# Performance work log

Measured on AMD Instinct MI355X. Metric: run time of the kernel, lower is better.

Reference implementation:

```python
import jax, jax.numpy as jnp
import numpy as np


def setup_inputs() -> dict:
    key = jax.random.key(0)
    k1, k2, k3, k4 = jax.random.split(key, 4)
    B, T, S, D = 256, 16, 32, 768
    return {
        "video_global": jax.random.normal(k1, (B, D), dtype=jnp.float32),
        "text_global": jax.random.normal(k2, (B, D), dtype=jnp.float32),
        "video_local": jax.random.normal(k3, (B, T, D), dtype=jnp.float32),
        "text_local": jax.random.normal(k4, (B, S, D), dtype=jnp.float32),
        "temp": jnp.zeros((1,), dtype=jnp.float32),  # log(1.0)
    }


def reference(video_global, text_global, video_local, text_local, temp):
    B = video_global.shape[0]
    logit_scale = jnp.exp(temp)[0]

    # ---- global contrastive loss ----
    global_sim = logit_scale * (video_global @ text_global.T)  # [B, B]
    diag = jnp.arange(B)
    loss_v2t = -jax.nn.log_softmax(global_sim, axis=1)[diag, diag].mean()
    loss_t2v = -jax.nn.log_softmax(global_sim, axis=0)[diag, diag].mean()
    loss_global = 0.5 * (loss_v2t + loss_t2v)

    # ---- local positive scores ----
    # paired (diagonal) local similarity: [B, T, S]
    sim_pos = logit_scale * jnp.einsum("btd,bsd->bts", video_local, text_local)
    time_weights = jax.nn.softmax(sim_pos.max(axis=-1), axis=-1)  # [B, T]
    pos_scores = (sim_pos.mean(axis=-1) * time_weights).sum(axis=1)  # [B]

    # ---- local negative scores (batched pairwise contraction) ----
    # [B, B, T, S]: video i vs text j, replacing the B*(B-1) tiny einsum loop
    sim_all = logit_scale * jnp.einsum("btd,csd->bcts", video_local, text_local)
    neg_full = (time_weights[:, None, :] * sim_all.mean(axis=-1)).sum(axis=-1)  # [B, B]

    # drop diagonal (i == j), preserving row-major loop order
    rows, cols = np.nonzero(~np.eye(B, dtype=bool))
    neg_scores = neg_full[rows, cols].reshape(B, B - 1)

    logits = jnp.concatenate([pos_scores[:, None], neg_scores], axis=-1)  # [B, B]
    loss_local = -jax.nn.log_softmax(logits, axis=-1)[:, 0].mean()

    return 0.6 * loss_global + 0.4 * loss_local
```

## Files before the change

### kernel.cpp

```cpp
#include <hip/hip_runtime.h>
#include <cmath>

#define BB 256
#define TT 16
#define SS 32
#define DD 768
#define LROW 260

__global__ __launch_bounds__(512) void hl_stage1(
    const float* __restrict__ vl, const float* __restrict__ tl,
    const float* __restrict__ temp,
    float* __restrict__ vw_ws, float* __restrict__ tb_ws)
{
    __shared__ float smem[12480];
    __shared__ float simb[512];
    __shared__ float rmax[16];
    __shared__ float twb[16];

    const int i   = blockIdx.x;
    const int tid = threadIdx.x;
    const float lsc = expf(temp[0]);

    const int slice = tid & 15;
    const int g     = tid >> 4;
    const int tg    = g >> 3;
    const int sg    = g & 7;

    const float* vli = vl + (size_t)i * TT * DD;
    const float* tli = tl + (size_t)i * SS * DD;

    float acc[4][4];
#pragma unroll
    for (int a = 0; a < 4; ++a)
#pragma unroll
        for (int b = 0; b < 4; ++b) acc[a][b] = 0.f;

    for (int c = 0; c < 3; ++c) {
        const int d0 = c << 8;
#pragma unroll
        for (int k = 0; k < 2; ++k) {
            int f4 = tid + (k << 9);
            int r  = f4 >> 6;
            int dc = (f4 & 63) << 2;
            *(float4*)&smem[r * LROW + dc] = *(const float4*)&vli[r * DD + d0 + dc];
        }
#pragma unroll
        for (int k = 0; k < 4; ++k) {
            int f4 = tid + (k << 9);
            int r  = f4 >> 6;
            int dc = (f4 & 63) << 2;
            *(float4*)&smem[(16 + r) * LROW + dc] = *(const float4*)&tli[r * DD + d0 + dc];
        }
        __syncthreads();
#pragma unroll
        for (int step = 0; step < 4; ++step) {
            const int db = (slice << 4) + (step << 2);
            float4 av[4], bv[4];
#pragma unroll
            for (int ti = 0; ti < 4; ++ti)
                av[ti] = *(const float4*)&smem[(tg * 4 + ti) * LROW + db];
#pragma unroll
            for (int sj = 0; sj < 4; ++sj)
                bv[sj] = *(const float4*)&smem[(16 + sg * 4 + sj) * LROW + db];
#pragma unroll
            for (int ti = 0; ti < 4; ++ti)
#pragma unroll
                for (int sj = 0; sj < 4; ++sj)
                    acc[ti][sj] += av[ti].x * bv[sj].x + av[ti].y * bv[sj].y
                                 + av[ti].z * bv[sj].z + av[ti].w * bv[sj].w;
        }
        __syncthreads();
    }

#pragma unroll
    for (int ti = 0; ti < 4; ++ti)
#pragma unroll
        for (int sj = 0; sj < 4; ++sj) {
            int t = tg * 4 + ti, s = sg * 4 + sj;
            smem[(t * 32 + s) * 17 + slice] = acc[ti][sj];
        }
    __syncthreads();
    {
        float ssum = 0.f;
#pragma unroll
        for (int k = 0; k < 16; ++k) ssum += smem[tid * 17 + k];
        simb[tid] = lsc * ssum;
    }
    __syncthreads();
    if (tid < 16) {
        float m = -3.0e38f;
        for (int s = 0; s < 32; ++s)
            m = fmaxf(m, simb[tid * 32 + ((s + tid) & 31)]);
        rmax[tid] = m;
    }
    __syncthreads();
    if (tid == 0) {
        float M = -3.0e38f;
        for (int t = 0; t < 16; ++t) M = fmaxf(M, rmax[t]);
        float ssum = 0.f;
        for (int t = 0; t < 16; ++t) {
            float e = expf(rmax[t] - M);
            twb[t] = e;
            ssum += e;
        }
        float inv = 1.0f / ssum;
        for (int t = 0; t < 16; ++t) twb[t] *= inv;
    }
    __syncthreads();

    for (int d = tid; d < DD; d += 512) {
        float vwv = 0.f;
#pragma unroll
        for (int t = 0; t < 16; ++t) vwv += twb[t] * vli[t * DD + d];
        vw_ws[(size_t)i * DD + d] = vwv;
        float tbv = 0.f;
#pragma unroll
        for (int s = 0; s < 32; ++s) tbv += tli[s * DD + d];
        tb_ws[(size_t)i * DD + d] = tbv * (1.0f / 32.0f);
    }
}

__global__ __launch_bounds__(256) void hl_gemm(
    const float* __restrict__ vg, const float* __restrict__ tg,
    const float* __restrict__ vw, const float* __restrict__ tb,
    const float* __restrict__ temp, float* __restrict__ cparts)
{
    __shared__ float As[16][68];
    __shared__ float Bs[16][68];
    __shared__ float Tb[64][68];

    const int b   = blockIdx.x;
    const int p   = b & 7;
    const int tj  = (b >> 3) & 3;
    const int ti  = (b >> 5) & 3;
    const int mat = b >> 7;
    const int tid = threadIdx.x;
    const float lsc = expf(temp[0]);

    const float* A  = mat ? vw : vg;
    const float* Bm = mat ? tb : tg;
    const int i0 = ti * 64, j0 = tj * 64, kb0 = p * 96;

    const int srow = tid >> 2, skq = tid & 3;
    const int tr = tid >> 4, tc = tid & 15;

    float acc[4][4];
#pragma unroll
    for (int r = 0; r < 4; ++r)
#pragma unroll
        for (int cc = 0; cc < 4; ++cc) acc[r][cc] = 0.f;

    for (int ch = 0; ch < 6; ++ch) {
        const int kb = kb0 + ch * 16;
        float4 a4 = *(const float4*)&A [(size_t)(i0 + srow) * DD + kb + skq * 4];
        float4 b4 = *(const float4*)&Bm[(size_t)(j0 + srow) * DD + kb + skq * 4];
        __syncthreads();
        As[skq * 4 + 0][srow] = a4.x; As[skq * 4 + 1][srow] = a4.y;
        As[skq * 4 + 2][srow] = a4.z; As[skq * 4 + 3][srow] = a4.w;
        Bs[skq * 4 + 0][srow] = b4.x; Bs[skq * 4 + 1][srow] = b4.y;
        Bs[skq * 4 + 2][srow] = b4.z; Bs[skq * 4 + 3][srow] = b4.w;
        __syncthreads();
#pragma unroll
        for (int k = 0; k < 16; ++k) {
            float4 av = *(const float4*)&As[k][tr * 4];
            float4 bv = *(const float4*)&Bs[k][tc * 4];
            float ar[4] = {av.x, av.y, av.z, av.w};
            float br[4] = {bv.x, bv.y, bv.z, bv.w};
#pragma unroll
            for (int r = 0; r < 4; ++r)
#pragma unroll
                for (int cc = 0; cc < 4; ++cc)
                    acc[r][cc] += ar[r] * br[cc];
        }
    }

    const int cm = mat ? 0 : 1;
    float* Cp = cparts + ((size_t)p * 3 + cm) * 65536;
#pragma unroll
    for (int r = 0; r < 4; ++r) {
        float4 v = {acc[r][0] * lsc, acc[r][1] * lsc, acc[r][2] * lsc, acc[r][3] * lsc};
        *(float4*)&Cp[(size_t)(i0 + tr * 4 + r) * 256 + j0 + tc * 4] = v;
    }
    if (mat == 0) {
        __syncthreads();
#pragma unroll
        for (int r = 0; r < 4; ++r)
#pragma unroll
            for (int cc = 0; cc < 4; ++cc)
                Tb[tc * 4 + cc][tr * 4 + r] = acc[r][cc] * lsc;
        __syncthreads();
        float* Ct = cparts + ((size_t)p * 3 + 2) * 65536;
#pragma unroll
        for (int r = 0; r < 4; ++r) {
            float4 v = *(const float4*)&Tb[tr * 4 + r][tc * 4];
            *(float4*)&Ct[(size_t)(j0 + tr * 4 + r) * 256 + i0 + tc * 4] = v;
        }
    }
}

__global__ __launch_bounds__(256) void hl_lse(
    const float* __restrict__ cparts, float* __restrict__ out)
{
    __shared__ float xs[256];
    __shared__ float wred[4];
    __shared__ float bcast;

    const int b   = blockIdx.x;
    const int cm  = b >> 8;
    const int row = b & 255;
    const int tid = threadIdx.x;

    float x = 0.f;
#pragma unroll
    for (int p = 0; p < 8; ++p)
        x += cparts[((size_t)p * 3 + cm) * 65536 + (size_t)row * 256 + tid];
    xs[tid] = x;

    float m = x;
#pragma unroll
    for (int off = 32; off > 0; off >>= 1)
        m = fmaxf(m, __shfl_down(m, off, 64));
    if ((tid & 63) == 0) wred[tid >> 6] = m;
    __syncthreads();
    if (tid == 0)
        bcast = fmaxf(fmaxf(wred[0], wred[1]), fmaxf(wred[2], wred[3]));
    __syncthreads();
    float M = bcast;
    float e = expf(x - M);
#pragma unroll
    for (int off = 32; off > 0; off >>= 1)
        e += __shfl_down(e, off, 64);
    if ((tid & 63) == 0) wred[tid >> 6] = e;
    __syncthreads();
    if (tid == 0) {
        float Stot = wred[0] + wred[1] + wred[2] + wred[3];
        float lse  = M + logf(Stot);
        float w    = (cm == 0) ? (0.4f / 256.0f) : (0.3f / 256.0f);
        atomicAdd(out, w * (lse - xs[row]));
    }
}

extern "C" void kernel_launch(void* const* d_in, const int* in_sizes, int n_in,
                              void* d_out, int out_size, void* d_ws, size_t ws_size,
                              hipStream_t stream)
{
    const float* vg   = (const float*)d_in[0];
    const float* tg   = (const float*)d_in[1];
    const float* vl   = (const float*)d_in[2];
    const float* tl   = (const float*)d_in[3];
    const float* temp = (const float*)d_in[4];
    float* out = (float*)d_out;

    float* vw     = (float*)d_ws;
    float* tb     = vw + (size_t)BB * DD;
    float* cparts = tb + (size_t)BB * DD;

    hipMemsetAsync(out, 0, sizeof(float) * out_size, stream);
    hl_stage1<<<dim3(BB),  dim3(512), 0, stream>>>(vl, tl, temp, vw, tb);
    hl_gemm  <<<dim3(256), dim3(256), 0, stream>>>(vg, tg, vw, tb, temp, cparts);
    hl_lse   <<<dim3(768), dim3(256), 0, stream>>>(cparts, out);
}
```

Measured before the change: 116.7 us.

## Prefetch tiles in registers, fuse text mean into staging, warp-per-row LSE, drop memset

Stage1 now prefetches the next 256-column chunk into registers while the current one is computed, and builds the text-token mean from the staged tiles instead of rereading text_local from global memory at the end. The GEMM kernel double-buffers its global loads in registers. The LSE kernel handles one row per wavefront with float4 loads and shuffle-only reductions, with no shared-memory round trips. The output memset is folded into block 0 of stage1, which removes one launch. The costs are higher register pressure and extra LDS for the partial-sum buffer, and block 0 has to zero the output before any later kernel adds to it.

```diff
diff --git a/kernel.cpp b/kernel.cpp
--- a/kernel.cpp
+++ b/kernel.cpp
@@ -10,21 +10,30 @@
 __global__ __launch_bounds__(512) void hl_stage1(
     const float* __restrict__ vl, const float* __restrict__ tl,
     const float* __restrict__ temp,
-    float* __restrict__ vw_ws, float* __restrict__ tb_ws)
-{
-    __shared__ float smem[12480];
-    __shared__ float simb[512];
-    __shared__ float rmax[16];
-    __shared__ float twb[16];
+    float* __restrict__ vw_ws, float* __restrict__ tb_ws,
+    float* __restrict__ out, int out_n)
+{
+    __shared__ float lds[15104];
+    float* smem  = lds;
+    float* tbacc = lds + 12480;
+    float* simb  = lds + 14560;
+    float* rmaxb = lds + 15072;
+    float* twb   = lds + 15088;
 
     const int i   = blockIdx.x;
     const int tid = threadIdx.x;
     const float lsc = expf(temp[0]);
+    if (i == 0) {
+        for (int o = tid; o < out_n; o += 512) out[o] = 0.f;
+    }
 
     const int slice = tid & 15;
     const int g     = tid >> 4;
-    const int tg    = g >> 3;
+    const int tgr   = g >> 3;
     const int sg    = g & 7;
+
+    const int r0 = tid >> 6;
+    const int dc = (tid & 63) << 2;
 
     const float* vli = vl + (size_t)i * TT * DD;
     const float* tli = tl + (size_t)i * SS * DD;
@@ -35,30 +44,42 @@
 #pragma unroll
         for (int b = 0; b < 4; ++b) acc[a][b] = 0.f;
 
+    float4 pv[2], pt[4];
+    pv[0] = *(const float4*)&vli[(r0    ) * DD + dc];
+    pv[1] = *(const float4*)&vli[(r0 + 8) * DD + dc];
+#pragma unroll
+    for (int k = 0; k < 4; ++k)
+        pt[k] = *(const float4*)&tli[(r0 + 8 * k) * DD + dc];
+
     for (int c = 0; c < 3; ++c) {
-        const int d0 = c << 8;
-#pragma unroll
-        for (int k = 0; k < 2; ++k) {
-            int f4 = tid + (k << 9);
-            int r  = f4 >> 6;
-            int dc = (f4 & 63) << 2;
-            *(float4*)&smem[r * LROW + dc] = *(const float4*)&vli[r * DD + d0 + dc];
-        }
-#pragma unroll
-        for (int k = 0; k < 4; ++k) {
-            int f4 = tid + (k << 9);
-            int r  = f4 >> 6;
-            int dc = (f4 & 63) << 2;
-            *(float4*)&smem[(16 + r) * LROW + dc] = *(const float4*)&tli[r * DD + d0 + dc];
-        }
-        __syncthreads();
+        *(float4*)&smem[(r0    ) * LROW + dc] = pv[0];
+        *(float4*)&smem[(r0 + 8) * LROW + dc] = pv[1];
+#pragma unroll
+        for (int k = 0; k < 4; ++k)
+            *(float4*)&smem[(16 + r0 + 8 * k) * LROW + dc] = pt[k];
+        {
+            float4 ps = {pt[0].x + pt[1].x + pt[2].x + pt[3].x,
+                         pt[0].y + pt[1].y + pt[2].y + pt[3].y,
+                         pt[0].z + pt[1].z + pt[2].z + pt[3].z,
+                         pt[0].w + pt[1].w + pt[2].w + pt[3].w};
+            *(float4*)&tbacc[r0 * LROW + dc] = ps;
+        }
+        __syncthreads();
+        if (c < 2) {
+            const int d0n = (c + 1) << 8;
+            pv[0] = *(const float4*)&vli[(r0    ) * DD + d0n + dc];
+            pv[1] = *(const float4*)&vli[(r0 + 8) * DD + d0n + dc];
+#pragma unroll
+            for (int k = 0; k < 4; ++k)
+                pt[k] = *(const float4*)&tli[(r0 + 8 * k) * DD + d0n + dc];
+        }
 #pragma unroll
         for (int step = 0; step < 4; ++step) {
             const int db = (slice << 4) + (step << 2);
             float4 av[4], bv[4];
 #pragma unroll
             for (int ti = 0; ti < 4; ++ti)
-                av[ti] = *(const float4*)&smem[(tg * 4 + ti) * LROW + db];
+                av[ti] = *(const float4*)&smem[(tgr * 4 + ti) * LROW + db];
 #pragma unroll
             for (int sj = 0; sj < 4; ++sj)
                 bv[sj] = *(const float4*)&smem[(16 + sg * 4 + sj) * LROW + db];
@@ -69,6 +90,12 @@
                     acc[ti][sj] += av[ti].x * bv[sj].x + av[ti].y * bv[sj].y
                                  + av[ti].z * bv[sj].z + av[ti].w * bv[sj].w;
         }
+        if (tid < 256) {
+            float s = 0.f;
+#pragma unroll
+            for (int j = 0; j < 8; ++j) s += tbacc[j * LROW + tid];
+            tb_ws[(size_t)i * DD + (c << 8) + tid] = s * (1.0f / 32.0f);
+        }
         __syncthreads();
     }
 
@@ -76,7 +103,7 @@
     for (int ti = 0; ti < 4; ++ti)
 #pragma unroll
         for (int sj = 0; sj < 4; ++sj) {
-            int t = tg * 4 + ti, s = sg * 4 + sj;
+            int t = tgr * 4 + ti, s = sg * 4 + sj;
             smem[(t * 32 + s) * 17 + slice] = acc[ti][sj];
         }
     __syncthreads();
@@ -91,15 +118,15 @@
         float m = -3.0e38f;
         for (int s = 0; s < 32; ++s)
             m = fmaxf(m, simb[tid * 32 + ((s + tid) & 31)]);
-        rmax[tid] = m;
+        rmaxb[tid] = m;
     }
     __syncthreads();
     if (tid == 0) {
         float M = -3.0e38f;
-        for (int t = 0; t < 16; ++t) M = fmaxf(M, rmax[t]);
+        for (int t = 0; t < 16; ++t) M = fmaxf(M, rmaxb[t]);
         float ssum = 0.f;
         for (int t = 0; t < 16; ++t) {
-            float e = expf(rmax[t] - M);
+            float e = expf(rmaxb[t] - M);
             twb[t] = e;
             ssum += e;
         }
@@ -113,10 +140,6 @@
 #pragma unroll
         for (int t = 0; t < 16; ++t) vwv += twb[t] * vli[t * DD + d];
         vw_ws[(size_t)i * DD + d] = vwv;
-        float tbv = 0.f;
-#pragma unroll
-        for (int s = 0; s < 32; ++s) tbv += tli[s * DD + d];
-        tb_ws[(size_t)i * DD + d] = tbv * (1.0f / 32.0f);
     }
 }
 
@@ -150,16 +173,21 @@
 #pragma unroll
         for (int cc = 0; cc < 4; ++cc) acc[r][cc] = 0.f;
 
+    float4 a4 = *(const float4*)&A [(size_t)(i0 + srow) * DD + kb0 + skq * 4];
+    float4 b4 = *(const float4*)&Bm[(size_t)(j0 + srow) * DD + kb0 + skq * 4];
+    float4 a4n = a4, b4n = b4;
     for (int ch = 0; ch < 6; ++ch) {
-        const int kb = kb0 + ch * 16;
-        float4 a4 = *(const float4*)&A [(size_t)(i0 + srow) * DD + kb + skq * 4];
-        float4 b4 = *(const float4*)&Bm[(size_t)(j0 + srow) * DD + kb + skq * 4];
         __syncthreads();
         As[skq * 4 + 0][srow] = a4.x; As[skq * 4 + 1][srow] = a4.y;
         As[skq * 4 + 2][srow] = a4.z; As[skq * 4 + 3][srow] = a4.w;
         Bs[skq * 4 + 0][srow] = b4.x; Bs[skq * 4 + 1][srow] = b4.y;
         Bs[skq * 4 + 2][srow] = b4.z; Bs[skq * 4 + 3][srow] = b4.w;
         __syncthreads();
+        if (ch < 5) {
+            const int kb = kb0 + (ch + 1) * 16;
+            a4n = *(const float4*)&A [(size_t)(i0 + srow) * DD + kb + skq * 4];
+            b4n = *(const float4*)&Bm[(size_t)(j0 + srow) * DD + kb + skq * 4];
+        }
 #pragma unroll
         for (int k = 0; k < 16; ++k) {
             float4 av = *(const float4*)&As[k][tr * 4];
@@ -172,6 +200,7 @@
                 for (int cc = 0; cc < 4; ++cc)
                     acc[r][cc] += ar[r] * br[cc];
         }
+        a4 = a4n; b4 = b4n;
     }
 
     const int cm = mat ? 0 : 1;
@@ -198,45 +227,35 @@
     }
 }
 
-__global__ __launch_bounds__(256) void hl_lse(
+__global__ __launch_bounds__(512) void hl_lse(
     const float* __restrict__ cparts, float* __restrict__ out)
 {
-    __shared__ float xs[256];
-    __shared__ float wred[4];
-    __shared__ float bcast;
-
-    const int b   = blockIdx.x;
-    const int cm  = b >> 8;
-    const int row = b & 255;
-    const int tid = threadIdx.x;
-
-    float x = 0.f;
-#pragma unroll
-    for (int p = 0; p < 8; ++p)
-        x += cparts[((size_t)p * 3 + cm) * 65536 + (size_t)row * 256 + tid];
-    xs[tid] = x;
-
-    float m = x;
+    const int rr   = (blockIdx.x << 3) + (threadIdx.x >> 6);
+    const int cm   = rr >> 8;
+    const int row  = rr & 255;
+    const int lane = threadIdx.x & 63;
+    const float w  = (cm == 0) ? (0.4f / 256.0f) : (0.3f / 256.0f);
+
+    float4 x = make_float4(0.f, 0.f, 0.f, 0.f);
+    const float* base = cparts + (size_t)cm * 65536 + (size_t)row * 256 + (lane << 2);
+#pragma unroll
+    for (int p = 0; p < 8; ++p) {
+        float4 v = *(const float4*)(base + (size_t)p * 3 * 65536);
+        x.x += v.x; x.y += v.y; x.z += v.z; x.w += v.w;
+    }
+    float m = fmaxf(fmaxf(x.x, x.y), fmaxf(x.z, x.w));
 #pragma unroll
     for (int off = 32; off > 0; off >>= 1)
-        m = fmaxf(m, __shfl_down(m, off, 64));
-    if ((tid & 63) == 0) wred[tid >> 6] = m;
-    __syncthreads();
-    if (tid == 0)
-        bcast = fmaxf(fmaxf(wred[0], wred[1]), fmaxf(wred[2], wred[3]));
-    __syncthreads();
-    float M = bcast;
-    float e = expf(x - M);
+        m = fmaxf(m, __shfl_xor(m, off, 64));
+    float e = expf(x.x - m) + expf(x.y - m) + expf(x.z - m) + expf(x.w - m);
 #pragma unroll
     for (int off = 32; off > 0; off >>= 1)
-        e += __shfl_down(e, off, 64);
-    if ((tid & 63) == 0) wred[tid >> 6] = e;
-    __syncthreads();
-    if (tid == 0) {
-        float Stot = wred[0] + wred[1] + wred[2] + wred[3];
-        float lse  = M + logf(Stot);
-        float w    = (cm == 0) ? (0.4f / 256.0f) : (0.3f / 256.0f);
-        atomicAdd(out, w * (lse - xs[row]));
+        e += __shfl_xor(e, off, 64);
+    if (lane == (row >> 2)) {
+        float lse = m + logf(e);
+        float xd = (row & 2) ? ((row & 1) ? x.w : x.z)
+                             : ((row & 1) ? x.y : x.x);
+        atomicAdd(out, w * (lse - xd));
     }
 }
 
@@ -252,11 +271,11 @@
     float* out = (float*)d_out;
 
     float* vw     = (float*)d_ws;
-    float* tb     = vw + (size_t)BB * DD;
-    float* cparts = tb + (size_t)BB * DD;
-
-    hipMemsetAsync(out, 0, sizeof(float) * out_size, stream);
-    hl_stage1<<<dim3(BB),  dim3(512), 0, stream>>>(vl, tl, temp, vw, tb);
-    hl_gemm  <<<dim3(256), dim3(256), 0, stream>>>(vg, tg, vw, tb, temp, cparts);
-    hl_lse   <<<dim3(768), dim3(256), 0, stream>>>(cparts, out);
-}
+    float* tbw    = vw + (size_t)BB * DD;
+    float* cparts = tbw + (size_t)BB * DD;
+
+    hl_stage1<<<dim3(BB),  dim3(512), 0, stream>>>(vl, tl, temp, vw, tbw,
+                                                   out, out_size);
+    hl_gemm  <<<dim3(256), dim3(256), 0, stream>>>(vg, tg, vw, tbw, temp, cparts);
+    hl_lse   <<<dim3(96),  dim3(512), 0, stream>>>(cparts, out);
+}
```

New measurement: 125.6 us. +7.6%, slower.
